# Kernel optimization log

Measured on AMD Instinct MI355X. Metric: run time of the kernel, lower is better.

## Reference

```python
import jax, jax.numpy as jnp
import numpy as np

N, D_IN, D_OUT, E = 8192, 1024, 1024, 8

def setup_inputs() -> dict:
    key = jax.random.key(0)
    ks = jax.random.split(key, 5)
    x = jax.random.normal(ks[0], (N, D_IN), dtype=jnp.float32)
    # expert weights stacked: [E, D_IN, D_OUT], bias [E, D_OUT]
    We = jax.random.normal(ks[1], (E, D_IN, D_OUT), dtype=jnp.float32) / np.sqrt(D_IN)
    be = jax.random.normal(ks[2], (E, D_OUT), dtype=jnp.float32) * 0.01
    # gating net: Linear(D_IN -> E)
    Wg = jax.random.normal(ks[3], (D_IN, E), dtype=jnp.float32) / np.sqrt(D_IN)
    bg = jax.random.normal(ks[4], (E,), dtype=jnp.float32) * 0.01
    return {"x": x, "We": We, "be": be, "Wg": Wg, "bg": bg}

def reference(x, We, be, Wg, bg):
    # gate: softmax over experts  [N, E]
    gate_probs = jax.nn.softmax(x @ Wg + bg, axis=-1)
    # all experts run densely on every token: [N, E, D_OUT]
    expert_out = jnp.einsum('ni,eio->neo', x, We) + be[None, :, :]
    # gate-weighted sum over experts: [N, D_OUT]
    return jnp.einsum('neo,ne->no', expert_out, gate_probs)
```

## Files before the change

kernel.cpp:

```cpp
#include <hip/hip_runtime.h>
#include <hip/hip_bf16.h>

#define N_TOK 8192
#define DIN   1024
#define DOUT  1024
#define NE    8
#define KTOT  (NE * DIN)
#define BM    256
#define BN    128
#define NKH   (KTOT / 32)

typedef __attribute__((ext_vector_type(4))) float f32x4;
typedef __attribute__((ext_vector_type(8))) short short8;
typedef unsigned int u32;

__device__ __forceinline__ ushort f2bf(float f) {
    u32 u = __float_as_uint(f);
    u32 r = (u + 0x7fffu + ((u >> 16) & 1u)) >> 16;
    return (ushort)r;
}

__device__ __forceinline__ void gload_lds16(const void* gp, void* lp) {
    __builtin_amdgcn_global_load_lds(
        (const __attribute__((address_space(1))) u32*)gp,
        (__attribute__((address_space(3))) u32*)lp, 16, 0, 0);
}

#define PH_BAR()    __builtin_amdgcn_s_barrier()
#define LGKM0()     asm volatile("s_waitcnt lgkmcnt(0)" ::: "memory")
#define VMCNT6()    asm volatile("s_waitcnt vmcnt(6)" ::: "memory")
#define VMCNT3()    asm volatile("s_waitcnt vmcnt(3)" ::: "memory")
#define VMCNT0()    asm volatile("s_waitcnt vmcnt(0)" ::: "memory")

__global__ void gate_kernel(const float* __restrict__ x, const float* __restrict__ Wg,
                            const float* __restrict__ bg, float* __restrict__ g) {
    int w = threadIdx.x >> 6, lane = threadIdx.x & 63;
    int n = blockIdx.x * 4 + w;
    const float* xr = x + (size_t)n * DIN;
    float p[NE];
#pragma unroll
    for (int e = 0; e < NE; ++e) p[e] = 0.f;
    for (int i = lane; i < DIN; i += 64) {
        float xv = xr[i];
        const float* wr_ = Wg + i * NE;
#pragma unroll
        for (int e = 0; e < NE; ++e) p[e] = fmaf(xv, wr_[e], p[e]);
    }
#pragma unroll
    for (int off = 32; off > 0; off >>= 1) {
#pragma unroll
        for (int e = 0; e < NE; ++e) p[e] += __shfl_down(p[e], off);
    }
    if (lane == 0) {
        float l2[NE], m = -1e30f;
#pragma unroll
        for (int e = 0; e < NE; ++e) { l2[e] = p[e] + bg[e]; m = fmaxf(m, l2[e]); }
        float s = 0.f;
#pragma unroll
        for (int e = 0; e < NE; ++e) { l2[e] = expf(l2[e] - m); s += l2[e]; }
        float inv = 1.f / s;
#pragma unroll
        for (int e = 0; e < NE; ++e) g[n * NE + e] = l2[e] * inv;
    }
}

__global__ void cvt_x_kernel(const float* __restrict__ x, ushort* __restrict__ xb) {
    int idx = blockIdx.x * 256 + threadIdx.x;
    float4 v = ((const float4*)x)[idx];
    ushort4 o = make_ushort4(f2bf(v.x), f2bf(v.y), f2bf(v.z), f2bf(v.w));
    ((ushort4*)xb)[idx] = o;
}

__global__ void transpose_w_kernel(const float* __restrict__ We, ushort* __restrict__ BT) {
    __shared__ float tile[64][65];
    int kb = blockIdx.x * 64, ob = blockIdx.y * 64;
    int t = threadIdx.x;
#pragma unroll
    for (int ph = 0; ph < 16; ++ph) {
        int idx = ph * 256 + t;
        int r = idx >> 6, c = idx & 63;
        tile[r][c] = We[(size_t)(kb + r) * DOUT + ob + c];
    }
    __syncthreads();
#pragma unroll
    for (int ph = 0; ph < 16; ++ph) {
        int idx = ph * 256 + t;
        int r = idx >> 6, c = idx & 63;
        BT[(size_t)(ob + r) * KTOT + kb + c] = f2bf(tile[c][r]);
    }
}

__global__ __launch_bounds__(512, 2) void moe_gemm(
    const ushort* __restrict__ xb,
    const ushort* __restrict__ BT,
    const float*  __restrict__ g,
    const float*  __restrict__ be,
    float*        __restrict__ out)
{
    __shared__ __align__(16) ushort Al[4][BM * 32];
    __shared__ __align__(16) ushort Bl[4][BN * 32];
    __shared__ __align__(16) float  gLds[BM][NE];

    int bid = blockIdx.x;
    int swz = (bid & 7) * 32 + (bid >> 3);
    int colb = swz & 7;
    int rowb = swz >> 3;
    int brow = rowb * BM, bcol = colb * BN;

    int tid = threadIdx.x;
    int w = tid >> 6, lane = tid & 63;
    int wm = w >> 1, wn = w & 1;
    int ro = lane & 15, gq = lane >> 4;
    int jrow = gq * 4;

    float4 gv = ((const float4*)(g + (size_t)brow * NE))[tid];
    ((float4*)&gLds[0][0])[tid] = gv;

    int offA[4], offB[4];
#pragma unroll
    for (int m = 0; m < 4; ++m) {
        int r = wm * 64 + m * 16 + ro;
        offA[m] = r * 32 + ((gq * 8) ^ ((r & 6) << 2));
    }
#pragma unroll
    for (int n = 0; n < 4; ++n) {
        int c = wn * 64 + n * 16 + ro;
        offB[n] = c * 32 + ((gq * 8) ^ ((c & 6) << 2));
    }

    auto stA = [&](int s, int K) {
#pragma unroll
        for (int L = 0; L < 2; ++L) {
            int chunk = L * 512 + tid;
            int row = chunk >> 2, slot = chunk & 3;
            int ks = (slot * 8) ^ ((row & 6) << 2);
            int ka = (K * 32) & (DIN - 1);
            gload_lds16(xb + (size_t)(brow + row) * DIN + ka + ks,
                        (char*)&Al[s][0] + (size_t)(chunk & ~63) * 16);
        }
    };
    auto stB = [&](int s, int K) {
        int chunk = tid;
        int row = chunk >> 2, slot = chunk & 3;
        int ks = (slot * 8) ^ ((row & 6) << 2);
        gload_lds16(BT + (size_t)(bcol + row) * KTOT + K * 32 + ks,
                    (char*)&Bl[s][0] + (size_t)(chunk & ~63) * 16);
    };

    f32x4 accP[4][4];
    u32   accB[4][4][2];
#pragma unroll
    for (int m = 0; m < 4; ++m)
#pragma unroll
        for (int n = 0; n < 4; ++n) {
            accP[m][n] = (f32x4){0.f, 0.f, 0.f, 0.f};
            accB[m][n][0] = 0u; accB[m][n][1] = 0u;
        }

    auto fold = [&](int e) {
#pragma unroll
        for (int m = 0; m < 4; ++m) {
            int rbase = wm * 64 + m * 16 + jrow;
            float g0 = gLds[rbase + 0][e], g1 = gLds[rbase + 1][e];
            float g2 = gLds[rbase + 2][e], g3 = gLds[rbase + 3][e];
#pragma unroll
            for (int n = 0; n < 4; ++n) {
                u32 p0 = accB[m][n][0];
                float lo0 = __uint_as_float(p0 << 16)         + g0 * accP[m][n][0];
                float hi0 = __uint_as_float(p0 & 0xffff0000u) + g1 * accP[m][n][1];
                accB[m][n][0] = (u32)f2bf(lo0) | ((u32)f2bf(hi0) << 16);
                u32 p1 = accB[m][n][1];
                float lo1 = __uint_as_float(p1 << 16)         + g2 * accP[m][n][2];
                float hi1 = __uint_as_float(p1 & 0xffff0000u) + g3 * accP[m][n][3];
                accB[m][n][1] = (u32)f2bf(lo1) | ((u32)f2bf(hi1) << 16);
                accP[m][n] = (f32x4){0.f, 0.f, 0.f, 0.f};
            }
        }
    };

    auto do_phase = [&](int k, bool issue) {
        const ushort* As = &Al[k & 3][0];
        const ushort* Bs = &Bl[k & 3][0];
        short8 a[4];
#pragma unroll
        for (int m = 0; m < 4; ++m) a[m] = *(const short8*)(As + offA[m]);
        short8 b0 = *(const short8*)(Bs + offB[0]);
        short8 b1 = *(const short8*)(Bs + offB[1]);
        short8 b2 = *(const short8*)(Bs + offB[2]);
        short8 b3 = *(const short8*)(Bs + offB[3]);
        if (issue) { stA((k + 3) & 3, k + 3); stB((k + 3) & 3, k + 3); }
        PH_BAR(); LGKM0();
        __builtin_amdgcn_s_setprio(1);
#pragma unroll
        for (int m = 0; m < 4; ++m) {
            accP[m][0] = __builtin_amdgcn_mfma_f32_16x16x32_bf16(a[m], b0, accP[m][0], 0, 0, 0);
            accP[m][1] = __builtin_amdgcn_mfma_f32_16x16x32_bf16(a[m], b1, accP[m][1], 0, 0, 0);
            accP[m][2] = __builtin_amdgcn_mfma_f32_16x16x32_bf16(a[m], b2, accP[m][2], 0, 0, 0);
            accP[m][3] = __builtin_amdgcn_mfma_f32_16x16x32_bf16(a[m], b3, accP[m][3], 0, 0, 0);
        }
        __builtin_amdgcn_s_setprio(0);
        if ((k & 31) == 31 && k != NKH - 1) fold(k >> 5);
    };

    stA(0, 0); stB(0, 0);
    stA(1, 1); stB(1, 1);
    stA(2, 2); stB(2, 2);
    VMCNT6();
    PH_BAR();

    for (int k = 0; k < NKH - 3; ++k) {
        do_phase(k, true);
        VMCNT6();
        PH_BAR();
    }
    do_phase(NKH - 3, false); VMCNT3(); PH_BAR();
    do_phase(NKH - 2, false); VMCNT0(); PH_BAR();
    do_phase(NKH - 1, false);

#pragma unroll
    for (int m = 0; m < 4; ++m) {
#pragma unroll
        for (int j = 0; j < 4; ++j) {
            int lrow = wm * 64 + m * 16 + jrow + j;
            int grow = brow + lrow;
            float g8[NE];
#pragma unroll
            for (int e = 0; e < NE; ++e) g8[e] = gLds[lrow][e];
#pragma unroll
            for (int n = 0; n < 4; ++n) {
                int col = bcol + wn * 64 + n * 16 + ro;
                float bias = 0.f;
#pragma unroll
                for (int e = 0; e < NE; ++e) bias = fmaf(g8[e], be[e * DOUT + col], bias);
                u32 p = accB[m][n][j >> 1];
                float base = __uint_as_float((j & 1) ? (p & 0xffff0000u) : (p << 16));
                out[(size_t)grow * DOUT + col] = base + g8[7] * accP[m][n][j] + bias;
            }
        }
    }
}

extern "C" void kernel_launch(void* const* d_in, const int* in_sizes, int n_in,
                              void* d_out, int out_size, void* d_ws, size_t ws_size,
                              hipStream_t stream) {
    const float* x  = (const float*)d_in[0];
    const float* We = (const float*)d_in[1];
    const float* be = (const float*)d_in[2];
    const float* Wg = (const float*)d_in[3];
    const float* bg = (const float*)d_in[4];
    float* out = (float*)d_out;

    char* ws = (char*)d_ws;
    float*  gbuf = (float*)ws;
    ushort* xb   = (ushort*)(ws + (size_t)256 * 1024);
    ushort* BT   = (ushort*)(ws + (size_t)256 * 1024 + (size_t)N_TOK * DIN * 2);

    gate_kernel<<<N_TOK / 4, 256, 0, stream>>>(x, Wg, bg, gbuf);
    cvt_x_kernel<<<(N_TOK * DIN / 4) / 256, 256, 0, stream>>>(x, xb);
    transpose_w_kernel<<<dim3(KTOT / 64, DOUT / 64), 256, 0, stream>>>(We, BT);
    moe_gemm<<<(N_TOK / BM) * (DOUT / BN), 512, 0, stream>>>(xb, BT, gbuf, be, out);
}
```

Measured before the change: 192.5 us.

## Double-buffer LDS fragments in registers and restructure main loop into 4-stage unroll

Main K loop is unrolled by four and fragment loads for the next stage go into a second register set, so MFMAs of stage k overlap the LDS reads of stage k+1. The wait counts change (lgkmcnt(8), vmcnt(3)) to match, and there is one barrier per stage instead of the barrier before each MFMA. The aim is to hide LDS read latency behind matrix math. In exchange, register pressure rises from the second fragment set, and the hand-tuned wait counts and buffer indices could race if they are off.

```diff
diff --git a/kernel.cpp b/kernel.cpp
--- a/kernel.cpp
+++ b/kernel.cpp
@@ -26,11 +26,11 @@
         (__attribute__((address_space(3))) u32*)lp, 16, 0, 0);
 }
 
-#define PH_BAR()    __builtin_amdgcn_s_barrier()
-#define LGKM0()     asm volatile("s_waitcnt lgkmcnt(0)" ::: "memory")
-#define VMCNT6()    asm volatile("s_waitcnt vmcnt(6)" ::: "memory")
-#define VMCNT3()    asm volatile("s_waitcnt vmcnt(3)" ::: "memory")
-#define VMCNT0()    asm volatile("s_waitcnt vmcnt(0)" ::: "memory")
+#define PH_BAR()  __builtin_amdgcn_s_barrier()
+#define LGKM0()   asm volatile("s_waitcnt lgkmcnt(0)" ::: "memory")
+#define LGKM8()   asm volatile("s_waitcnt lgkmcnt(8)" ::: "memory")
+#define VMCNT3()  asm volatile("s_waitcnt vmcnt(3)" ::: "memory")
+#define VMCNT0()  asm volatile("s_waitcnt vmcnt(0)" ::: "memory")
 
 __global__ void gate_kernel(const float* __restrict__ x, const float* __restrict__ Wg,
                             const float* __restrict__ bg, float* __restrict__ g) {
@@ -149,6 +149,7 @@
 
     f32x4 accP[4][4];
     u32   accB[4][4][2];
+    short8 fA[2][4], fB[2][4];
 #pragma unroll
     for (int m = 0; m < 4; ++m)
 #pragma unroll
@@ -178,44 +179,57 @@
         }
     };
 
-    auto do_phase = [&](int k, bool issue) {
-        const ushort* As = &Al[k & 3][0];
-        const ushort* Bs = &Bl[k & 3][0];
-        short8 a[4];
-#pragma unroll
-        for (int m = 0; m < 4; ++m) a[m] = *(const short8*)(As + offA[m]);
-        short8 b0 = *(const short8*)(Bs + offB[0]);
-        short8 b1 = *(const short8*)(Bs + offB[1]);
-        short8 b2 = *(const short8*)(Bs + offB[2]);
-        short8 b3 = *(const short8*)(Bs + offB[3]);
-        if (issue) { stA((k + 3) & 3, k + 3); stB((k + 3) & 3, k + 3); }
-        PH_BAR(); LGKM0();
-        __builtin_amdgcn_s_setprio(1);
-#pragma unroll
-        for (int m = 0; m < 4; ++m) {
-            accP[m][0] = __builtin_amdgcn_mfma_f32_16x16x32_bf16(a[m], b0, accP[m][0], 0, 0, 0);
-            accP[m][1] = __builtin_amdgcn_mfma_f32_16x16x32_bf16(a[m], b1, accP[m][1], 0, 0, 0);
-            accP[m][2] = __builtin_amdgcn_mfma_f32_16x16x32_bf16(a[m], b2, accP[m][2], 0, 0, 0);
-            accP[m][3] = __builtin_amdgcn_mfma_f32_16x16x32_bf16(a[m], b3, accP[m][3], 0, 0, 0);
-        }
-        __builtin_amdgcn_s_setprio(0);
-        if ((k & 31) == 31 && k != NKH - 1) fold(k >> 5);
-    };
+#define LD_FRAGS(SET, RBUF) do {                                              \
+    const ushort* _As = &Al[RBUF][0];                                         \
+    const ushort* _Bs = &Bl[RBUF][0];                                         \
+    _Pragma("unroll") for (int _m = 0; _m < 4; ++_m)                          \
+        fA[SET][_m] = *(const short8*)(_As + offA[_m]);                       \
+    _Pragma("unroll") for (int _n = 0; _n < 4; ++_n)                          \
+        fB[SET][_n] = *(const short8*)(_Bs + offB[_n]);                       \
+} while (0)
+
+#define DO_MFMA(SET) do {                                                     \
+    __builtin_amdgcn_s_setprio(1);                                            \
+    _Pragma("unroll") for (int _m = 0; _m < 4; ++_m) {                        \
+        accP[_m][0] = __builtin_amdgcn_mfma_f32_16x16x32_bf16(fA[SET][_m], fB[SET][0], accP[_m][0], 0, 0, 0); \
+        accP[_m][1] = __builtin_amdgcn_mfma_f32_16x16x32_bf16(fA[SET][_m], fB[SET][1], accP[_m][1], 0, 0, 0); \
+        accP[_m][2] = __builtin_amdgcn_mfma_f32_16x16x32_bf16(fA[SET][_m], fB[SET][2], accP[_m][2], 0, 0, 0); \
+        accP[_m][3] = __builtin_amdgcn_mfma_f32_16x16x32_bf16(fA[SET][_m], fB[SET][3], accP[_m][3], 0, 0, 0); \
+    }                                                                         \
+    __builtin_amdgcn_s_setprio(0);                                            \
+} while (0)
 
     stA(0, 0); stB(0, 0);
     stA(1, 1); stB(1, 1);
     stA(2, 2); stB(2, 2);
-    VMCNT6();
+    VMCNT3();
     PH_BAR();
-
-    for (int k = 0; k < NKH - 3; ++k) {
-        do_phase(k, true);
-        VMCNT6();
-        PH_BAR();
-    }
-    do_phase(NKH - 3, false); VMCNT3(); PH_BAR();
-    do_phase(NKH - 2, false); VMCNT0(); PH_BAR();
-    do_phase(NKH - 1, false);
+    LD_FRAGS(0, 0);
+
+    for (int it = 0; it < 63; ++it) {
+        int k = it * 4;
+        LD_FRAGS(1, 1); stA(3, k + 3); stB(3, k + 3);
+        LGKM8(); DO_MFMA(0); VMCNT3(); PH_BAR();
+        LD_FRAGS(0, 2); stA(0, k + 4); stB(0, k + 4);
+        LGKM8(); DO_MFMA(1); VMCNT3(); PH_BAR();
+        LD_FRAGS(1, 3); stA(1, k + 5); stB(1, k + 5);
+        LGKM8(); DO_MFMA(0); VMCNT3(); PH_BAR();
+        LD_FRAGS(0, 0); stA(2, k + 6); stB(2, k + 6);
+        LGKM8(); DO_MFMA(1);
+        if ((it & 7) == 7) fold(it >> 3);
+        VMCNT3(); PH_BAR();
+    }
+
+    LD_FRAGS(1, 1); stA(3, 255); stB(3, 255);
+    LGKM8(); DO_MFMA(0); VMCNT3(); PH_BAR();
+    LD_FRAGS(0, 2);
+    LGKM8(); DO_MFMA(1); VMCNT0(); PH_BAR();
+    LD_FRAGS(1, 3);
+    LGKM8(); DO_MFMA(0); PH_BAR();
+    LGKM0(); DO_MFMA(1);
+
+#undef LD_FRAGS
+#undef DO_MFMA
 
 #pragma unroll
     for (int m = 0; m < 4; ++m) {
```

Result: slower. 197.7 us (+2.7%).

## Prescale activations by gate probs into bf16 A matrix and simplify GEMM

Applied to the files above, without the earlier changes.

Adds a prescale kernel that writes a gate-weighted bf16 copy of x, one block per expert (N x 8K), so the expert mixing becomes a plain GEMM against the transposed weights. A separate kernel initializes the output with the gate-weighted bias, and the simplified GEMM uses 3-stage buffering, no fold logic and higher occupancy, then accumulates into the output. This removes the in-kernel per-expert fold and epilogue work, but writes and reads a 128 MB scaled activation buffer and adds a read-modify-write of the output. The old path is kept as a fallback when the workspace is too small.

```diff
diff --git a/kernel.cpp b/kernel.cpp
--- a/kernel.cpp
+++ b/kernel.cpp
@@ -8,7 +8,6 @@
 #define KTOT  (NE * DIN)
 #define BM    256
 #define BN    128
-#define NKH   (KTOT / 32)
 
 typedef __attribute__((ext_vector_type(4))) float f32x4;
 typedef __attribute__((ext_vector_type(8))) short short8;
@@ -26,11 +25,11 @@
         (__attribute__((address_space(3))) u32*)lp, 16, 0, 0);
 }
 
-#define PH_BAR()    __builtin_amdgcn_s_barrier()
-#define LGKM0()     asm volatile("s_waitcnt lgkmcnt(0)" ::: "memory")
-#define VMCNT6()    asm volatile("s_waitcnt vmcnt(6)" ::: "memory")
-#define VMCNT3()    asm volatile("s_waitcnt vmcnt(3)" ::: "memory")
-#define VMCNT0()    asm volatile("s_waitcnt vmcnt(0)" ::: "memory")
+#define PH_BAR()  __builtin_amdgcn_s_barrier()
+#define LGKM0()   asm volatile("s_waitcnt lgkmcnt(0)" ::: "memory")
+#define VMCNT6()  asm volatile("s_waitcnt vmcnt(6)" ::: "memory")
+#define VMCNT3()  asm volatile("s_waitcnt vmcnt(3)" ::: "memory")
+#define VMCNT0()  asm volatile("s_waitcnt vmcnt(0)" ::: "memory")
 
 __global__ void gate_kernel(const float* __restrict__ x, const float* __restrict__ Wg,
                             const float* __restrict__ bg, float* __restrict__ g) {
@@ -64,6 +63,166 @@
     }
 }
 
+__global__ void transpose_w_kernel(const float* __restrict__ We, ushort* __restrict__ BT) {
+    __shared__ float tile[64][65];
+    int kb = blockIdx.x * 64, ob = blockIdx.y * 64;
+    int t = threadIdx.x;
+#pragma unroll
+    for (int ph = 0; ph < 16; ++ph) {
+        int idx = ph * 256 + t;
+        int r = idx >> 6, c = idx & 63;
+        tile[r][c] = We[(size_t)(kb + r) * DOUT + ob + c];
+    }
+    __syncthreads();
+#pragma unroll
+    for (int ph = 0; ph < 16; ++ph) {
+        int idx = ph * 256 + t;
+        int r = idx >> 6, c = idx & 63;
+        BT[(size_t)(ob + r) * KTOT + kb + c] = f2bf(tile[c][r]);
+    }
+}
+
+__global__ void prescale_kernel(const float* __restrict__ x, const float* __restrict__ g,
+                                ushort* __restrict__ Ag) {
+    int idx = blockIdx.x * 256 + threadIdx.x;
+    int n = idx >> 7, c = idx & 127;
+    float4 x0 = *(const float4*)&x[(size_t)n * DIN + c * 8];
+    float4 x1 = *(const float4*)&x[(size_t)n * DIN + c * 8 + 4];
+    float4 g0 = *(const float4*)&g[(size_t)n * NE + 0];
+    float4 g1 = *(const float4*)&g[(size_t)n * NE + 4];
+    float ge[NE] = {g0.x, g0.y, g0.z, g0.w, g1.x, g1.y, g1.z, g1.w};
+#pragma unroll
+    for (int e = 0; e < NE; ++e) {
+        float s = ge[e];
+        short8 v;
+        v[0] = (short)f2bf(s * x0.x); v[1] = (short)f2bf(s * x0.y);
+        v[2] = (short)f2bf(s * x0.z); v[3] = (short)f2bf(s * x0.w);
+        v[4] = (short)f2bf(s * x1.x); v[5] = (short)f2bf(s * x1.y);
+        v[6] = (short)f2bf(s * x1.z); v[7] = (short)f2bf(s * x1.w);
+        *(short8*)&Ag[(size_t)n * KTOT + e * DIN + c * 8] = v;
+    }
+}
+
+__global__ void biasinit_kernel(const float* __restrict__ g, const float* __restrict__ be,
+                                float* __restrict__ out) {
+    int idx = blockIdx.x * 256 + threadIdx.x;
+    int n = idx >> 8, o4 = (idx & 255) * 4;
+    float4 g0 = *(const float4*)&g[(size_t)n * NE + 0];
+    float4 g1 = *(const float4*)&g[(size_t)n * NE + 4];
+    float ge[NE] = {g0.x, g0.y, g0.z, g0.w, g1.x, g1.y, g1.z, g1.w};
+    f32x4 acc = (f32x4){0.f, 0.f, 0.f, 0.f};
+#pragma unroll
+    for (int e = 0; e < NE; ++e) {
+        f32x4 b = *(const f32x4*)&be[e * DOUT + o4];
+        acc += ge[e] * b;
+    }
+    *(f32x4*)&out[(size_t)n * DOUT + o4] = acc;
+}
+
+__global__ __launch_bounds__(512, 4) void moe_gemm_ps(
+    const ushort* __restrict__ Ag,
+    const ushort* __restrict__ BT,
+    float*        __restrict__ out)
+{
+    __shared__ __align__(16) ushort Al[3][BM * 32];
+    __shared__ __align__(16) ushort Bl[3][BN * 32];
+
+    int bid = blockIdx.x;
+    int swz = (bid & 7) * 32 + (bid >> 3);
+    int colb = swz & 7;
+    int rowb = swz >> 3;
+    int brow = rowb * BM, bcol = colb * BN;
+
+    int tid = threadIdx.x;
+    int w = tid >> 6, lane = tid & 63;
+    int wm = w >> 1, wn = w & 1;
+    int ro = lane & 15, gq = lane >> 4;
+
+    int offA[4], offB[4];
+#pragma unroll
+    for (int m = 0; m < 4; ++m) {
+        int r = wm * 64 + m * 16 + ro;
+        offA[m] = r * 32 + ((gq * 8) ^ ((r & 6) << 2));
+    }
+#pragma unroll
+    for (int n = 0; n < 4; ++n) {
+        int c = wn * 64 + n * 16 + ro;
+        offB[n] = c * 32 + ((gq * 8) ^ ((c & 6) << 2));
+    }
+
+    auto stage = [&](int s, int K) {
+#pragma unroll
+        for (int L = 0; L < 2; ++L) {
+            int chunk = L * 512 + tid;
+            int row = chunk >> 2, slot = chunk & 3;
+            int ks = (slot * 8) ^ ((row & 6) << 2);
+            gload_lds16(Ag + (size_t)(brow + row) * KTOT + K * 32 + ks,
+                        (char*)&Al[s][0] + (size_t)(chunk & ~63) * 16);
+        }
+        int chunk = tid;
+        int row = chunk >> 2, slot = chunk & 3;
+        int ks = (slot * 8) ^ ((row & 6) << 2);
+        gload_lds16(BT + (size_t)(bcol + row) * KTOT + K * 32 + ks,
+                    (char*)&Bl[s][0] + (size_t)(chunk & ~63) * 16);
+    };
+
+    f32x4 accP[4][4];
+#pragma unroll
+    for (int m = 0; m < 4; ++m)
+#pragma unroll
+        for (int n = 0; n < 4; ++n) accP[m][n] = (f32x4){0.f, 0.f, 0.f, 0.f};
+
+#define PHASE(BUF, SBUF, KK, ISSUE, WAITN) do {                               \
+    const ushort* _As = &Al[BUF][0];                                          \
+    const ushort* _Bs = &Bl[BUF][0];                                          \
+    short8 _a[4], _b[4];                                                      \
+    _Pragma("unroll") for (int _m = 0; _m < 4; ++_m)                          \
+        _a[_m] = *(const short8*)(_As + offA[_m]);                            \
+    _Pragma("unroll") for (int _n = 0; _n < 4; ++_n)                          \
+        _b[_n] = *(const short8*)(_Bs + offB[_n]);                            \
+    if (ISSUE) stage(SBUF, (KK) + 2);                                         \
+    __builtin_amdgcn_s_setprio(1);                                            \
+    _Pragma("unroll") for (int _m = 0; _m < 4; ++_m) {                        \
+        accP[_m][0] = __builtin_amdgcn_mfma_f32_16x16x32_bf16(_a[_m], _b[0], accP[_m][0], 0, 0, 0); \
+        accP[_m][1] = __builtin_amdgcn_mfma_f32_16x16x32_bf16(_a[_m], _b[1], accP[_m][1], 0, 0, 0); \
+        accP[_m][2] = __builtin_amdgcn_mfma_f32_16x16x32_bf16(_a[_m], _b[2], accP[_m][2], 0, 0, 0); \
+        accP[_m][3] = __builtin_amdgcn_mfma_f32_16x16x32_bf16(_a[_m], _b[3], accP[_m][3], 0, 0, 0); \
+    }                                                                         \
+    __builtin_amdgcn_s_setprio(0);                                            \
+    if ((WAITN) == 3) VMCNT3(); else if ((WAITN) == 0) VMCNT0();              \
+    if ((WAITN) >= 0) PH_BAR();                                               \
+} while (0)
+
+    stage(0, 0); stage(1, 1);
+    VMCNT3();
+    PH_BAR();
+
+    for (int it = 0; it < 84; ++it) {
+        int k = it * 3;
+        PHASE(0, 2, k + 0, 1, 3);
+        PHASE(1, 0, k + 1, 1, 3);
+        PHASE(2, 1, k + 2, 1, 3);
+    }
+    PHASE(0, 2, 252, 1, 3);
+    PHASE(1, 0, 253, 1, 3);
+    PHASE(2, 0, 254, 0, 0);
+    PHASE(0, 0, 255, 0, -1);
+#undef PHASE
+
+#pragma unroll
+    for (int m = 0; m < 4; ++m) {
+#pragma unroll
+        for (int j = 0; j < 4; ++j) {
+            int grow = brow + wm * 64 + m * 16 + gq * 4 + j;
+#pragma unroll
+            for (int n = 0; n < 4; ++n) {
+                int col = bcol + wn * 64 + n * 16 + ro;
+                out[(size_t)grow * DOUT + col] += accP[m][n][j];
+            }
+        }
+    }
+}
+
 __global__ void cvt_x_kernel(const float* __restrict__ x, ushort* __restrict__ xb) {
     int idx = blockIdx.x * 256 + threadIdx.x;
     float4 v = ((const float4*)x)[idx];
@@ -71,31 +230,10 @@
     ((ushort4*)xb)[idx] = o;
 }
 
-__global__ void transpose_w_kernel(const float* __restrict__ We, ushort* __restrict__ BT) {
-    __shared__ float tile[64][65];
-    int kb = blockIdx.x * 64, ob = blockIdx.y * 64;
-    int t = threadIdx.x;
-#pragma unroll
-    for (int ph = 0; ph < 16; ++ph) {
-        int idx = ph * 256 + t;
-        int r = idx >> 6, c = idx & 63;
-        tile[r][c] = We[(size_t)(kb + r) * DOUT + ob + c];
-    }
-    __syncthreads();
-#pragma unroll
-    for (int ph = 0; ph < 16; ++ph) {
-        int idx = ph * 256 + t;
-        int r = idx >> 6, c = idx & 63;
-        BT[(size_t)(ob + r) * KTOT + kb + c] = f2bf(tile[c][r]);
-    }
-}
-
-__global__ __launch_bounds__(512, 2) void moe_gemm(
-    const ushort* __restrict__ xb,
-    const ushort* __restrict__ BT,
-    const float*  __restrict__ g,
-    const float*  __restrict__ be,
-    float*        __restrict__ out)
+__global__ __launch_bounds__(512, 2) void moe_gemm_fb(
+    const ushort* __restrict__ xb, const ushort* __restrict__ BT,
+    const float* __restrict__ g, const float* __restrict__ be,
+    float* __restrict__ out)
 {
     __shared__ __align__(16) ushort Al[4][BM * 32];
     __shared__ __align__(16) ushort Bl[4][BN * 32];
@@ -103,10 +241,8 @@
 
     int bid = blockIdx.x;
     int swz = (bid & 7) * 32 + (bid >> 3);
-    int colb = swz & 7;
-    int rowb = swz >> 3;
+    int colb = swz & 7, rowb = swz >> 3;
     int brow = rowb * BM, bcol = colb * BN;
-
     int tid = threadIdx.x;
     int w = tid >> 6, lane = tid & 63;
     int wm = w >> 1, wn = w & 1;
@@ -199,7 +335,7 @@
             accP[m][3] = __builtin_amdgcn_mfma_f32_16x16x32_bf16(a[m], b3, accP[m][3], 0, 0, 0);
         }
         __builtin_amdgcn_s_setprio(0);
-        if ((k & 31) == 31 && k != NKH - 1) fold(k >> 5);
+        if ((k & 31) == 31 && k != 255) fold(k >> 5);
     };
 
     stA(0, 0); stB(0, 0);
@@ -208,14 +344,14 @@
     VMCNT6();
     PH_BAR();
 
-    for (int k = 0; k < NKH - 3; ++k) {
+    for (int k = 0; k < 253; ++k) {
         do_phase(k, true);
         VMCNT6();
         PH_BAR();
     }
-    do_phase(NKH - 3, false); VMCNT3(); PH_BAR();
-    do_phase(NKH - 2, false); VMCNT0(); PH_BAR();
-    do_phase(NKH - 1, false);
+    do_phase(253, false); VMCNT3(); PH_BAR();
+    do_phase(254, false); VMCNT0(); PH_BAR();
+    do_phase(255, false);
 
 #pragma unroll
     for (int m = 0; m < 4; ++m) {
@@ -251,12 +387,26 @@
     float* out = (float*)d_out;
 
     char* ws = (char*)d_ws;
-    float*  gbuf = (float*)ws;
-    ushort* xb   = (ushort*)(ws + (size_t)256 * 1024);
-    ushort* BT   = (ushort*)(ws + (size_t)256 * 1024 + (size_t)N_TOK * DIN * 2);
-
+    const size_t GB   = 256 * 1024;
+    const size_t BTB  = (size_t)DOUT * KTOT * 2;
+    const size_t AGB  = (size_t)N_TOK * KTOT * 2;
+    const size_t NEED = GB + BTB + AGB;
+
+    float* gbuf = (float*)ws;
     gate_kernel<<<N_TOK / 4, 256, 0, stream>>>(x, Wg, bg, gbuf);
-    cvt_x_kernel<<<(N_TOK * DIN / 4) / 256, 256, 0, stream>>>(x, xb);
-    transpose_w_kernel<<<dim3(KTOT / 64, DOUT / 64), 256, 0, stream>>>(We, BT);
-    moe_gemm<<<(N_TOK / BM) * (DOUT / BN), 512, 0, stream>>>(xb, BT, gbuf, be, out);
-}
+
+    if (ws_size >= NEED) {
+        ushort* BT = (ushort*)(ws + GB);
+        ushort* Ag = (ushort*)(ws + GB + BTB);
+        transpose_w_kernel<<<dim3(KTOT / 64, DOUT / 64), 256, 0, stream>>>(We, BT);
+        prescale_kernel<<<(N_TOK * 128) / 256, 256, 0, stream>>>(x, gbuf, Ag);
+        biasinit_kernel<<<(N_TOK * 256) / 256, 256, 0, stream>>>(gbuf, be, out);
+        moe_gemm_ps<<<(N_TOK / BM) * (DOUT / BN), 512, 0, stream>>>(Ag, BT, out);
+    } else {
+        ushort* xb = (ushort*)(ws + GB);
+        ushort* BT = (ushort*)(ws + GB + (size_t)N_TOK * DIN * 2);
+        cvt_x_kernel<<<(N_TOK * DIN / 4) / 256, 256, 0, stream>>>(x, xb);
+        transpose_w_kernel<<<dim3(KTOT / 64, DOUT / 64), 256, 0, stream>>>(We, BT);
+        moe_gemm_fb<<<(N_TOK / BM) * (DOUT / BN), 512, 0, stream>>>(xb, BT, gbuf, be, out);
+    }
+}
```

After: 217.0 us. 1.13x slower.
